# Kernel optimization log

Hardware: AMD Instinct MI355X
Metric: run time of the kernel (lower is better)

## Reference

```python
import jax, jax.numpy as jnp
import numpy as np

EPSILON = 0.05


def _l2_normalize(x, axis=1, eps=1e-12):
    return x / jnp.maximum(jnp.linalg.norm(x, axis=axis, keepdims=True), eps)


def _pairwise_euclidean_distance(a, b):
    # [N, d], [K, d] -> [N, K] euclidean distances (torch.cdist semantics)
    sq = (jnp.sum(a * a, axis=1)[:, None]
          + jnp.sum(b * b, axis=1)[None, :]
          - 2.0 * (a @ b.T))
    return jnp.sqrt(jnp.maximum(sq, 1e-12))


def _sinkhorn(out, epsilon):
    # Faithful to the original: the loop body never updates Q, so the result
    # is a single row-then-column normalization regardless of `iterations`.
    Q = jnp.exp(out / epsilon).T              # [K, B]
    K, B = Q.shape
    Q = Q / jnp.sum(Q)
    Q1 = Q / jnp.sum(Q, axis=1, keepdims=True) / K
    Q2 = Q1 / jnp.sum(Q1, axis=0, keepdims=True) / B
    return (Q2 * B).T                          # [B, K]


def _cross_entropy(x1, x2):
    return -jnp.mean(jnp.sum(x1 * jnp.log(x2), axis=1))


def setup_inputs() -> dict:
    key = jax.random.key(0)
    k1, k2, k3 = jax.random.split(key, 3)
    two_bsz, d, K = 32768, 256, 1024
    return {
        "z": jax.random.normal(k1, (two_bsz, d), dtype=jnp.float32),
        "p": jax.random.normal(k2, (two_bsz, d), dtype=jnp.float32),
        "centers": jax.random.normal(k3, (K, d), dtype=jnp.float32),
    }


def reference(z, p, centers):
    z = _l2_normalize(z, axis=1)
    p = _l2_normalize(p, axis=1)
    c = _l2_normalize(centers, axis=1)

    bsz = z.shape[0] // 2
    z1, z2 = z[:bsz], z[bsz:]
    p1, p2 = p[:bsz], p[bsz:]

    za_1 = _sinkhorn(_pairwise_euclidean_distance(z1, c), EPSILON)
    za_2 = _sinkhorn(_pairwise_euclidean_distance(z2, c), EPSILON)
    pa_1 = _sinkhorn(_pairwise_euclidean_distance(p1, c), EPSILON)
    pa_2 = _sinkhorn(_pairwise_euclidean_distance(p2, c), EPSILON)

    # cls_use_both_views = True
    return (_cross_entropy(za_1, pa_1) + _cross_entropy(za_1, pa_2)
            + _cross_entropy(za_2, pa_1) + _cross_entropy(za_2, pa_2)) / 4.0
```

## Files before the change

### kernel.cpp

```cpp
#include <hip/hip_runtime.h>
#include <math.h>

#define BH  16384
#define B2  32768
#define DIM 256
#define KC  1024

typedef __bf16 bf16x8 __attribute__((ext_vector_type(8)));
typedef float  f32x4  __attribute__((ext_vector_type(4)));

__device__ __forceinline__ unsigned short f2bf(float f) {
  unsigned int u = __float_as_uint(f);
  u += 0x7FFFu + ((u >> 16) & 1u);
  return (unsigned short)(u >> 16);
}

__device__ __forceinline__ float vsqrt(float x) {
  float r; asm("v_sqrt_f32 %0, %1" : "=v"(r) : "v"(x)); return r;
}

__device__ __forceinline__ void gld_lds16(const void* g, void* l) {
  __builtin_amdgcn_global_load_lds(
      (const __attribute__((address_space(1))) void*)g,
      (__attribute__((address_space(3))) void*)l, 16, 0, 0);
}

__global__ void norm_rows_kernel(const float* __restrict__ z,
                                 const float* __restrict__ p,
                                 const float* __restrict__ c,
                                 unsigned short* __restrict__ Xn,
                                 unsigned short* __restrict__ Cn,
                                 float* __restrict__ colsum,
                                 float* __restrict__ out) {
  if (blockIdx.x < 16) colsum[blockIdx.x * 256 + threadIdx.x] = 0.0f;
  if (blockIdx.x == 16 && threadIdx.x == 0) out[0] = 0.0f;

  int wave = threadIdx.x >> 6;
  int lane = threadIdx.x & 63;
  int row  = blockIdx.x * 4 + wave;
  const float* src; unsigned short* dst; int r;
  if (row < B2)        { src = z; dst = Xn; r = row; }
  else if (row < 2*B2) { src = p; dst = Xn + (size_t)B2 * DIM; r = row - B2; }
  else                 { src = c; dst = Cn; r = row - 2*B2; }
  float4 v = *reinterpret_cast<const float4*>(src + (size_t)r * DIM + lane * 4);
  float ss = v.x*v.x + v.y*v.y + v.z*v.z + v.w*v.w;
  #pragma unroll
  for (int m = 1; m < 64; m <<= 1) ss += __shfl_xor(ss, m);
  float inv = 1.0f / fmaxf(vsqrt(ss), 1e-12f);
  ushort4 o;
  o.x = f2bf(v.x * inv); o.y = f2bf(v.y * inv);
  o.z = f2bf(v.z * inv); o.w = f2bf(v.w * inv);
  *reinterpret_cast<ushort4*>(dst + (size_t)r * DIM + lane * 4) = o;
}

__global__ void fin_logC_kernel(const float* __restrict__ colsum,
                                float* __restrict__ logC) {
  int i = blockIdx.x * 256 + threadIdx.x;
  if (i < 4 * KC) logC[i] = 40.0f + __logf(colsum[i]);
}

__global__ __launch_bounds__(256, 2)
void gemm_s_kernel(const unsigned short* __restrict__ XA,
                   const unsigned short* __restrict__ Cn,
                   float* __restrict__ colsum,
                   unsigned char* __restrict__ S) {
  __shared__ __align__(16) char lds[65536 + 4096];
  float* lut4 = (float*)(lds + 65536);
  const int id  = blockIdx.x;
  const int xcd = id & 7, idx = id >> 3;
  const int wk  = xcd * 128 + idx;
  const int panel = wk >> 3, col = wk & 7;
  const int tm0 = panel * 128, tn0 = col * 128;

  const int tid  = threadIdx.x;
  const int lane = tid & 63;
  const int wid  = tid >> 6;
  const int wm   = wid >> 1, wn = wid & 1;
  const int l15  = lane & 15, l4 = lane >> 4;
  const int slot = tid & 3;

  int arow[4], acs[4];
  #pragma unroll
  for (int it = 0; it < 4; ++it) {
    int sl = it * 256 + tid;
    int r = sl >> 3, c = sl & 7;
    arow[it] = r;
    acs[it]  = c ^ (r & 7);
  }
  const char* Abase = (const char*)XA + (size_t)tm0 * 512;
  const char* Bbase = (const char*)Cn + (size_t)tn0 * 512;

  auto stage = [&](int t) {
    const int mat = t >> 2;
    const int bk  = t & 3;
    const int b   = t & 1;
    const char* ab = Abase + ((size_t)mat << 23);
    #pragma unroll
    for (int it = 0; it < 4; ++it) {
      gld_lds16(ab + (size_t)arow[it] * 512 + bk * 128 + acs[it] * 16,
                lds + b * 16384 + (it * 256 + tid) * 16);
      gld_lds16(Bbase + (size_t)arow[it] * 512 + bk * 128 + acs[it] * 16,
                lds + 32768 + b * 16384 + (it * 256 + tid) * 16);
    }
  };

  if (tid < 256) {
    float d = ((float)tid - 127.5f) * (1.0f / 255.0f);
    float L = 20.0f * vsqrt(2.0f - 2.0f * d);
    float v = __expf(L - 40.0f);
    ((float4*)lut4)[tid] = (float4){v, v, v, v};
  }

  f32x4 acc[4][4];
  stage(0);
  __syncthreads();

  for (int t = 0; t < 16; ++t) {
    if (t < 15) stage(t + 1);
    const int b  = t & 1;
    const int mat = t >> 2, bk = t & 3;

    if (bk == 0) {
      #pragma unroll
      for (int fi = 0; fi < 4; ++fi)
        #pragma unroll
        for (int fj = 0; fj < 4; ++fj)
          acc[fi][fj] = (f32x4){0.f, 0.f, 0.f, 0.f};
    }

    #pragma unroll
    for (int kc = 0; kc < 2; ++kc) {
      bf16x8 aF[4], bF[4];
      #pragma unroll
      for (int f = 0; f < 4; ++f) {
        const int ra = wm * 64 + f * 16 + l15;
        aF[f] = *reinterpret_cast<const bf16x8*>(
            lds + b * 16384 + ra * 128 + ((((kc << 2) | l4) ^ (ra & 7)) << 4));
        const int rb = wn * 64 + f * 16 + l15;
        bF[f] = *reinterpret_cast<const bf16x8*>(
            lds + 32768 + b * 16384 + rb * 128 + ((((kc << 2) | l4) ^ (rb & 7)) << 4));
      }
      #pragma unroll
      for (int fi = 0; fi < 4; ++fi)
        #pragma unroll
        for (int fj = 0; fj < 4; ++fj)
          acc[fi][fj] = __builtin_amdgcn_mfma_f32_16x16x32_bf16(
              aF[fi], bF[fj], acc[fi][fj], 0, 0, 0);
    }

    if (bk == 3) {
      unsigned char* Sp = S + ((size_t)mat * BH + tm0) * KC + tn0;
      #pragma unroll
      for (int fj = 0; fj < 4; ++fj) {
        float cp = 0.0f;
        #pragma unroll
        for (int fi = 0; fi < 4; ++fi)
          #pragma unroll
          for (int i = 0; i < 4; ++i) {
            float v = fmaf(acc[fi][fj][i], 255.0f, 128.0f);
            v = fminf(fmaxf(v, 0.0f), 255.0f);
            unsigned e = (unsigned)v;
            cp += lut4[(e << 2) | slot];
            int row  = wm * 64 + fi * 16 + l4 * 4 + i;
            int ccol = wn * 64 + fj * 16 + l15;
            Sp[(size_t)row * KC + ccol] = (unsigned char)e;
          }
        cp += __shfl_xor(cp, 16);
        cp += __shfl_xor(cp, 32);
        if (l4 == 0)
          atomicAdd(&colsum[mat * KC + tn0 + wn * 64 + fj * 16 + l15], cp);
      }
    }
    __syncthreads();
  }
}

__device__ __forceinline__ float decG(unsigned e, float lc) {
  float d = fmaf((float)e, 1.0f / 255.0f, -0.5f);
  float L = 20.0f * vsqrt(fmaf(-2.0f, d, 2.0f));
  return L - lc;
}

__global__ __launch_bounds__(256)
void pass2_mem_kernel(const unsigned char* __restrict__ S,
                      const float* __restrict__ logC,
                      float* __restrict__ rowv) {
  const int tid  = threadIdx.x;
  const int lane = tid & 63;
  const int wid  = tid >> 6;
  const int row  = blockIdx.x * 4 + wid;
  const size_t plane = (size_t)BH * KC;
  const unsigned char* Sr = S + (size_t)row * KC;

  float dp1 = 0.f, dp2 = 0.f, dz1 = 0.f, dz2 = 0.f, nz1 = 0.f, nz2 = 0.f;

  #pragma unroll
  for (int it = 0; it < 2; ++it) {
    const int kb = it * 512 + lane * 8;
    uint2 vz1 = *reinterpret_cast<const uint2*>(Sr + 0 * plane + kb);
    uint2 vz2 = *reinterpret_cast<const uint2*>(Sr + 1 * plane + kb);
    uint2 vp1 = *reinterpret_cast<const uint2*>(Sr + 2 * plane + kb);
    uint2 vp2 = *reinterpret_cast<const uint2*>(Sr + 3 * plane + kb);

    float cz1[8], cz2[8], cp1[8], cp2[8];
    *reinterpret_cast<float4*>(&cz1[0]) = *reinterpret_cast<const float4*>(logC + 0 * KC + kb);
    *reinterpret_cast<float4*>(&cz1[4]) = *reinterpret_cast<const float4*>(logC + 0 * KC + kb + 4);
    *reinterpret_cast<float4*>(&cz2[0]) = *reinterpret_cast<const float4*>(logC + 1 * KC + kb);
    *reinterpret_cast<float4*>(&cz2[4]) = *reinterpret_cast<const float4*>(logC + 1 * KC + kb + 4);
    *reinterpret_cast<float4*>(&cp1[0]) = *reinterpret_cast<const float4*>(logC + 2 * KC + kb);
    *reinterpret_cast<float4*>(&cp1[4]) = *reinterpret_cast<const float4*>(logC + 2 * KC + kb + 4);
    *reinterpret_cast<float4*>(&cp2[0]) = *reinterpret_cast<const float4*>(logC + 3 * KC + kb);
    *reinterpret_cast<float4*>(&cp2[4]) = *reinterpret_cast<const float4*>(logC + 3 * KC + kb + 4);

    unsigned b1[8], b2[8];
    #pragma unroll
    for (int e = 0; e < 4; ++e) {
      b1[e]     = (vp1.x >> (8 * e)) & 0xffu;
      b1[e + 4] = (vp1.y >> (8 * e)) & 0xffu;
      b2[e]     = (vp2.x >> (8 * e)) & 0xffu;
      b2[e + 4] = (vp2.y >> (8 * e)) & 0xffu;
    }
    float tv[8];
    #pragma unroll
    for (int e = 0; e < 8; ++e) {
      float g1 = decG(b1[e], cp1[e]);
      float g2 = decG(b2[e], cp2[e]);
      dp1 += __expf(g1);
      dp2 += __expf(g2);
      tv[e] = g1 + g2;
    }
    #pragma unroll
    for (int e = 0; e < 4; ++e) {
      b1[e]     = (vz1.x >> (8 * e)) & 0xffu;
      b1[e + 4] = (vz1.y >> (8 * e)) & 0xffu;
      b2[e]     = (vz2.x >> (8 * e)) & 0xffu;
      b2[e + 4] = (vz2.y >> (8 * e)) & 0xffu;
    }
    #pragma unroll
    for (int e = 0; e < 8; ++e) {
      float e1 = __expf(decG(b1[e], cz1[e]));
      float e2 = __expf(decG(b2[e], cz2[e]));
      dz1 += e1; nz1 += e1 * tv[e];
      dz2 += e2; nz2 += e2 * tv[e];
    }
  }

  #pragma unroll
  for (int m = 1; m < 64; m <<= 1) {
    dp1 += __shfl_xor(dp1, m); dp2 += __shfl_xor(dp2, m);
    dz1 += __shfl_xor(dz1, m); dz2 += __shfl_xor(dz2, m);
    nz1 += __shfl_xor(nz1, m); nz2 += __shfl_xor(nz2, m);
  }

  __shared__ float red[4];
  if (lane == 0)
    red[wid] = nz1 / dz1 + nz2 / dz2 - 2.0f * (__logf(dp1) + __logf(dp2));
  __syncthreads();
  if (tid == 0)
    rowv[blockIdx.x] = red[0] + red[1] + red[2] + red[3];
}

__global__ void fin_reduce_kernel(const float* __restrict__ rowv,
                                  float* __restrict__ out) {
  int i = blockIdx.x * 256 + threadIdx.x;
  float v = rowv[i];
  #pragma unroll
  for (int m = 1; m < 64; m <<= 1) v += __shfl_xor(v, m);
  __shared__ float ws[4];
  int lane = threadIdx.x & 63, wid = threadIdx.x >> 6;
  if (lane == 0) ws[wid] = v;
  __syncthreads();
  if (threadIdx.x == 0)
    atomicAdd(out, (ws[0] + ws[1] + ws[2] + ws[3]) * (-1.0f / 65536.0f));
}

extern "C" void kernel_launch(void* const* d_in, const int* in_sizes, int n_in,
                              void* d_out, int out_size, void* d_ws, size_t ws_size,
                              hipStream_t stream) {
  const float* z = (const float*)d_in[0];
  const float* p = (const float*)d_in[1];
  const float* c = (const float*)d_in[2];
  char* ws = (char*)d_ws;
  unsigned short* Xn = (unsigned short*)(ws);
  unsigned short* Cn = (unsigned short*)(ws + 33554432);
  float* colsum = (float*)(ws + 34078720);
  float* logC   = (float*)(ws + 34095104);
  float* rowv   = (float*)(ws + 34111488);
  unsigned char* S = (unsigned char*)(ws + 34127872);
  float* out = (float*)d_out;

  norm_rows_kernel<<<16640, 256, 0, stream>>>(z, p, c, Xn, Cn, colsum, out);
  gemm_s_kernel<<<1024, 256, 0, stream>>>(Xn, Cn, colsum, S);
  fin_logC_kernel<<<16, 256, 0, stream>>>(colsum, logC);
  pass2_mem_kernel<<<4096, 256, 0, stream>>>(S, logC, rowv);
  fin_reduce_kernel<<<16, 256, 0, stream>>>(rowv, out);
}
```

Measured before the change: 107.8 us.

## Rewrite GEMM as 256x256 tile, 8-wave kernel with interleaved load/MFMA schedule

Replaces the 128x128 four-wave GEMM with a 256x256 eight-wave kernel that uses 128KB of LDS and a hand-scheduled pipeline. Global-to-LDS loads for later tiles are interleaved with MFMA quadrants, separated by explicit barriers, sched_barriers, setprio and vmcnt waits. Larger tiles raise operand reuse and the explicit schedule aims to overlap memory traffic with matrix math. The launch drops to 256 blocks, which could leave the GPU underfilled. The manual waitcnt and barrier choreography is fragile and could hide race conditions.

```diff
diff --git a/kernel.cpp b/kernel.cpp
--- a/kernel.cpp
+++ b/kernel.cpp
@@ -59,50 +59,31 @@
   if (i < 4 * KC) logC[i] = 40.0f + __logf(colsum[i]);
 }
 
-__global__ __launch_bounds__(256, 2)
-void gemm_s_kernel(const unsigned short* __restrict__ XA,
-                   const unsigned short* __restrict__ Cn,
-                   float* __restrict__ colsum,
-                   unsigned char* __restrict__ S) {
-  __shared__ __align__(16) char lds[65536 + 4096];
-  float* lut4 = (float*)(lds + 65536);
-  const int id  = blockIdx.x;
-  const int xcd = id & 7, idx = id >> 3;
-  const int wk  = xcd * 128 + idx;
-  const int panel = wk >> 3, col = wk & 7;
-  const int tm0 = panel * 128, tn0 = col * 128;
+
+#define SBAR() __builtin_amdgcn_sched_barrier(0)
+#define BARR() __builtin_amdgcn_s_barrier()
+#define VM6()  asm volatile("s_waitcnt vmcnt(6)" ::: "memory")
+
+__global__ __launch_bounds__(512, 2)
+void gemm8_kernel(const unsigned short* __restrict__ XA,
+                  const unsigned short* __restrict__ Cn,
+                  float* __restrict__ colsum,
+                  unsigned char* __restrict__ S) {
+  __shared__ __align__(16) char lds[135168];
+  float* lut4 = (float*)(lds + 131072);
+
+  const int id = blockIdx.x;
+  const int wk = (id & 7) * 32 + (id >> 3);
+  const int panel = wk >> 2, col = wk & 3;
+  const int tm0 = panel * 256, tn0 = col * 256;
 
   const int tid  = threadIdx.x;
   const int lane = tid & 63;
   const int wid  = tid >> 6;
-  const int wm   = wid >> 1, wn = wid & 1;
+  const int wm   = wid >> 2, wn = wid & 3;
   const int l15  = lane & 15, l4 = lane >> 4;
-  const int slot = tid & 3;
-
-  int arow[4], acs[4];
-  #pragma unroll
-  for (int it = 0; it < 4; ++it) {
-    int sl = it * 256 + tid;
-    int r = sl >> 3, c = sl & 7;
-    arow[it] = r;
-    acs[it]  = c ^ (r & 7);
-  }
-  const char* Abase = (const char*)XA + (size_t)tm0 * 512;
-  const char* Bbase = (const char*)Cn + (size_t)tn0 * 512;
-
-  auto stage = [&](int t) {
-    const int mat = t >> 2;
-    const int bk  = t & 3;
-    const int b   = t & 1;
-    const char* ab = Abase + ((size_t)mat << 23);
-    #pragma unroll
-    for (int it = 0; it < 4; ++it) {
-      gld_lds16(ab + (size_t)arow[it] * 512 + bk * 128 + acs[it] * 16,
-                lds + b * 16384 + (it * 256 + tid) * 16);
-      gld_lds16(Bbase + (size_t)arow[it] * 512 + bk * 128 + acs[it] * 16,
-                lds + 32768 + b * 16384 + (it * 256 + tid) * 16);
-    }
-  };
+  const int sw   = l15 & 7;
+  const int slot4 = tid & 3;
 
   if (tid < 256) {
     float d = ((float)tid - 127.5f) * (1.0f / 255.0f);
@@ -111,57 +92,134 @@
     ((float4*)lut4)[tid] = (float4){v, v, v, v};
   }
 
-  f32x4 acc[4][4];
-  stage(0);
+  const int srow0 = tid >> 3,          sc0 = (tid & 7) ^ (srow0 & 7);
+  const int srow1 = srow0 + 64,        sc1 = ((tid + 512) & 7) ^ (srow1 & 7);
+
+#define ST_A(tile, half, dst) do {                                          \
+    int tt_ = (tile) & 15;                                                  \
+    const char* src_ = (const char*)XA + ((size_t)(tt_ >> 2) << 23)         \
+        + (size_t)(tm0 + (half) * 128) * 512 + (tt_ & 3) * 128;             \
+    gld_lds16(src_ + (size_t)srow0 * 512 + sc0 * 16,                        \
+              lds + (dst) + tid * 16);                                      \
+    gld_lds16(src_ + (size_t)srow1 * 512 + sc1 * 16,                        \
+              lds + (dst) + (tid + 512) * 16);                              \
+  } while (0)
+
+#define ST_B(tile, half, dst) do {                                          \
+    int tt_ = (tile) & 15;                                                  \
+    const char* src_ = (const char*)Cn                                      \
+        + (size_t)(tn0 + (half) * 128) * 512 + (tt_ & 3) * 128;             \
+    gld_lds16(src_ + (size_t)srow0 * 512 + sc0 * 16,                        \
+              lds + (dst) + tid * 16);                                      \
+    gld_lds16(src_ + (size_t)srow1 * 512 + sc1 * 16,                        \
+              lds + (dst) + (tid + 512) * 16);                              \
+  } while (0)
+
+  bf16x8 aR[8], bR0[4], bR1[4];
+  f32x4  acc[8][4];
+
+#define RD_A(base, ah) do {                                                 \
+    _Pragma("unroll")                                                       \
+    for (int f_ = 0; f_ < 4; ++f_) {                                        \
+      int ra_ = wm * 128 + (ah) * 64 + f_ * 16 + l15;                       \
+      _Pragma("unroll")                                                     \
+      for (int kc_ = 0; kc_ < 2; ++kc_)                                     \
+        aR[f_ * 2 + kc_] = *(const bf16x8*)(lds + (base) + ra_ * 128        \
+            + (((kc_ * 4 + l4) ^ sw) << 4));                                \
+    }                                                                       \
+  } while (0)
+
+#define RD_B(base, bh, bR) do {                                             \
+    _Pragma("unroll")                                                       \
+    for (int g_ = 0; g_ < 2; ++g_) {                                        \
+      int rb_ = wn * 64 + (bh) * 32 + g_ * 16 + l15;                        \
+      _Pragma("unroll")                                                     \
+      for (int kc_ = 0; kc_ < 2; ++kc_)                                     \
+        bR[g_ * 2 + kc_] = *(const bf16x8*)(lds + (base) + rb_ * 128        \
+            + (((kc_ * 4 + l4) ^ sw) << 4));                                \
+    }                                                                       \
+  } while (0)
+
+#define QUAD(ah, bh, bR) do {                                               \
+    _Pragma("unroll")                                                       \
+    for (int kc_ = 0; kc_ < 2; ++kc_)                                       \
+      _Pragma("unroll")                                                     \
+      for (int f_ = 0; f_ < 4; ++f_)                                        \
+        _Pragma("unroll")                                                   \
+        for (int g_ = 0; g_ < 2; ++g_)                                      \
+          acc[(ah) * 4 + f_][(bh) * 2 + g_] =                               \
+              __builtin_amdgcn_mfma_f32_16x16x32_bf16(                      \
+                  aR[f_ * 2 + kc_], bR[g_ * 2 + kc_],                       \
+                  acc[(ah) * 4 + f_][(bh) * 2 + g_], 0, 0, 0);              \
+  } while (0)
+
+#define SYNC_MFMA(ah, bh, bR) do {                                          \
+    SBAR(); BARR(); SBAR();                                                 \
+    __builtin_amdgcn_s_setprio(1);                                          \
+    QUAD(ah, bh, bR);                                                       \
+    __builtin_amdgcn_s_setprio(0);                                          \
+    SBAR(); BARR();                                                         \
+  } while (0)
+
+  ST_A(0, 0, 0);            ST_A(0, 1, 16384);
+  ST_B(0, 0, 65536);        ST_B(0, 1, 65536 + 16384);
+  ST_A(1, 0, 32768);
+  ST_B(1, 0, 65536 + 32768);
+  ST_B(1, 1, 65536 + 32768 + 16384);
   __syncthreads();
 
-  for (int t = 0; t < 16; ++t) {
-    if (t < 15) stage(t + 1);
-    const int b  = t & 1;
-    const int mat = t >> 2, bk = t & 3;
-
-    if (bk == 0) {
+  #pragma unroll 1
+  for (int it = 0; it < 8; ++it) {
+    const int t0 = 2 * it, t1 = t0 + 1;
+
+    if ((it & 1) == 0) {
       #pragma unroll
-      for (int fi = 0; fi < 4; ++fi)
+      for (int fi = 0; fi < 8; ++fi)
         #pragma unroll
         for (int fj = 0; fj < 4; ++fj)
           acc[fi][fj] = (f32x4){0.f, 0.f, 0.f, 0.f};
     }
 
-    #pragma unroll
-    for (int kc = 0; kc < 2; ++kc) {
-      bf16x8 aF[4], bF[4];
-      #pragma unroll
-      for (int f = 0; f < 4; ++f) {
-        const int ra = wm * 64 + f * 16 + l15;
-        aF[f] = *reinterpret_cast<const bf16x8*>(
-            lds + b * 16384 + ra * 128 + ((((kc << 2) | l4) ^ (ra & 7)) << 4));
-        const int rb = wn * 64 + f * 16 + l15;
-        bF[f] = *reinterpret_cast<const bf16x8*>(
-            lds + 32768 + b * 16384 + rb * 128 + ((((kc << 2) | l4) ^ (rb & 7)) << 4));
-      }
-      #pragma unroll
-      for (int fi = 0; fi < 4; ++fi)
-        #pragma unroll
-        for (int fj = 0; fj < 4; ++fj)
-          acc[fi][fj] = __builtin_amdgcn_mfma_f32_16x16x32_bf16(
-              aF[fi], bF[fj], acc[fi][fj], 0, 0, 0);
-    }
-
-    if (bk == 3) {
+    RD_B(65536, 0, bR0); RD_A(0, 0);
+    ST_A(t1, 1, 32768 + 16384);
+    SYNC_MFMA(0, 0, bR0);
+    RD_B(65536, 1, bR1);
+    ST_A(t0 + 2, 0, 0);
+    SYNC_MFMA(0, 1, bR1);
+    RD_A(0, 1);
+    ST_B(t0 + 2, 0, 65536);
+    SYNC_MFMA(1, 1, bR1);
+    ST_B(t0 + 2, 1, 65536 + 16384);
+    VM6();
+    SYNC_MFMA(1, 0, bR0);
+    RD_B(65536 + 32768, 0, bR0); RD_A(32768, 0);
+    ST_A(t0 + 2, 1, 16384);
+    SYNC_MFMA(0, 0, bR0);
+    RD_B(65536 + 32768, 1, bR1);
+    ST_A(t1 + 2, 0, 32768);
+    SYNC_MFMA(0, 1, bR1);
+    RD_A(32768, 1);
+    ST_B(t1 + 2, 0, 65536 + 32768);
+    SYNC_MFMA(1, 1, bR1);
+    ST_B(t1 + 2, 1, 65536 + 32768 + 16384);
+    VM6();
+    SYNC_MFMA(1, 0, bR0);
+
+    if (it & 1) {
+      const int mat = it >> 1;
       unsigned char* Sp = S + ((size_t)mat * BH + tm0) * KC + tn0;
       #pragma unroll
       for (int fj = 0; fj < 4; ++fj) {
         float cp = 0.0f;
         #pragma unroll
-        for (int fi = 0; fi < 4; ++fi)
+        for (int fi = 0; fi < 8; ++fi)
           #pragma unroll
           for (int i = 0; i < 4; ++i) {
             float v = fmaf(acc[fi][fj][i], 255.0f, 128.0f);
             v = fminf(fmaxf(v, 0.0f), 255.0f);
             unsigned e = (unsigned)v;
-            cp += lut4[(e << 2) | slot];
-            int row  = wm * 64 + fi * 16 + l4 * 4 + i;
+            cp += lut4[(e << 2) | slot4];
+            int row  = wm * 128 + fi * 16 + l4 * 4 + i;
             int ccol = wn * 64 + fj * 16 + l15;
             Sp[(size_t)row * KC + ccol] = (unsigned char)e;
           }
@@ -170,8 +228,8 @@
         if (l4 == 0)
           atomicAdd(&colsum[mat * KC + tn0 + wn * 64 + fj * 16 + l15], cp);
       }
-    }
-    __syncthreads();
+      VM6();
+    }
   }
 }
 
@@ -290,7 +348,7 @@
   float* out = (float*)d_out;
 
   norm_rows_kernel<<<16640, 256, 0, stream>>>(z, p, c, Xn, Cn, colsum, out);
-  gemm_s_kernel<<<1024, 256, 0, stream>>>(Xn, Cn, colsum, S);
+  gemm8_kernel<<<256, 512, 0, stream>>>(Xn, Cn, colsum, S);
   fin_logC_kernel<<<16, 256, 0, stream>>>(colsum, logC);
   pass2_mem_kernel<<<4096, 256, 0, stream>>>(S, logC, rowv);
   fin_reduce_kernel<<<16, 256, 0, stream>>>(rowv, out);
```

Result: slower. 244.5 us (+126.9%).

## Halve GEMM K-tile and LDS to raise occupancy, hoist pass2 loads

Applied to the files above, without the earlier changes.

The GEMM K-step drops from 64 to 32 elements per stage, which shrinks LDS from about 68KB to 40KB. Launch bounds rise to 4 blocks per CU to hide latency, the swizzle is adapted, and the LUT is widened to 8 slots to cut bank conflicts. In pass2, all eight byte loads per row are issued up front before the compute, to raise memory-level parallelism. The trade-off is twice as many barriers and stage steps in the GEMM, plus a tighter register budget that may cause spills.

```diff
diff --git a/kernel.cpp b/kernel.cpp
--- a/kernel.cpp
+++ b/kernel.cpp
@@ -59,13 +59,13 @@
   if (i < 4 * KC) logC[i] = 40.0f + __logf(colsum[i]);
 }
 
-__global__ __launch_bounds__(256, 2)
+__global__ __launch_bounds__(256, 4)
 void gemm_s_kernel(const unsigned short* __restrict__ XA,
                    const unsigned short* __restrict__ Cn,
                    float* __restrict__ colsum,
                    unsigned char* __restrict__ S) {
-  __shared__ __align__(16) char lds[65536 + 4096];
-  float* lut4 = (float*)(lds + 65536);
+  __shared__ __align__(16) char lds[40960];
+  float* lut8 = (float*)(lds + 32768);
   const int id  = blockIdx.x;
   const int xcd = id & 7, idx = id >> 3;
   const int wk  = xcd * 128 + idx;
@@ -77,50 +77,48 @@
   const int wid  = tid >> 6;
   const int wm   = wid >> 1, wn = wid & 1;
   const int l15  = lane & 15, l4 = lane >> 4;
-  const int slot = tid & 3;
-
-  int arow[4], acs[4];
-  #pragma unroll
-  for (int it = 0; it < 4; ++it) {
-    int sl = it * 256 + tid;
-    int r = sl >> 3, c = sl & 7;
-    arow[it] = r;
-    acs[it]  = c ^ (r & 7);
-  }
-  const char* Abase = (const char*)XA + (size_t)tm0 * 512;
-  const char* Bbase = (const char*)Cn + (size_t)tn0 * 512;
-
-  auto stage = [&](int t) {
-    const int mat = t >> 2;
-    const int bk  = t & 3;
-    const int b   = t & 1;
-    const char* ab = Abase + ((size_t)mat << 23);
-    #pragma unroll
-    for (int it = 0; it < 4; ++it) {
-      gld_lds16(ab + (size_t)arow[it] * 512 + bk * 128 + acs[it] * 16,
-                lds + b * 16384 + (it * 256 + tid) * 16);
-      gld_lds16(Bbase + (size_t)arow[it] * 512 + bk * 128 + acs[it] * 16,
-                lds + 32768 + b * 16384 + (it * 256 + tid) * 16);
-    }
-  };
-
-  if (tid < 256) {
+  const int l7   = lane & 7;
+
+  {
     float d = ((float)tid - 127.5f) * (1.0f / 255.0f);
     float L = 20.0f * vsqrt(2.0f - 2.0f * d);
     float v = __expf(L - 40.0f);
-    ((float4*)lut4)[tid] = (float4){v, v, v, v};
-  }
+    ((float4*)lut8)[tid * 2]     = (float4){v, v, v, v};
+    ((float4*)lut8)[tid * 2 + 1] = (float4){v, v, v, v};
+  }
+
+  int arow[2], acs[2];
+  #pragma unroll
+  for (int it = 0; it < 2; ++it) {
+    int slot = it * 256 + tid;
+    arow[it] = slot >> 2;
+    acs[it]  = (slot & 3) ^ (arow[it] & 3);
+  }
+  const char* Abase = (const char*)XA + (size_t)tm0 * 512;
+  const char* Bbase = (const char*)Cn + (size_t)tn0 * 512;
+
+  auto stage = [&](int t) {
+    const int mat = t >> 3, bk = t & 7, b = t & 1;
+    const char* ab = Abase + ((size_t)mat << 23);
+    #pragma unroll
+    for (int it = 0; it < 2; ++it) {
+      gld_lds16(ab + (size_t)arow[it] * 512 + bk * 64 + acs[it] * 16,
+                lds + b * 8192 + (it * 256 + tid) * 16);
+      gld_lds16(Bbase + (size_t)arow[it] * 512 + bk * 64 + acs[it] * 16,
+                lds + 16384 + b * 8192 + (it * 256 + tid) * 16);
+    }
+  };
 
   f32x4 acc[4][4];
   stage(0);
   __syncthreads();
 
-  for (int t = 0; t < 16; ++t) {
-    if (t < 15) stage(t + 1);
-    const int b  = t & 1;
-    const int mat = t >> 2, bk = t & 3;
-
-    if (bk == 0) {
+  #pragma unroll 1
+  for (int t = 0; t < 32; ++t) {
+    if (t < 31) stage(t + 1);
+    const int b = t & 1;
+
+    if ((t & 7) == 0) {
       #pragma unroll
       for (int fi = 0; fi < 4; ++fi)
         #pragma unroll
@@ -128,27 +126,25 @@
           acc[fi][fj] = (f32x4){0.f, 0.f, 0.f, 0.f};
     }
 
-    #pragma unroll
-    for (int kc = 0; kc < 2; ++kc) {
-      bf16x8 aF[4], bF[4];
+    bf16x8 aF[4], bF[4];
+    #pragma unroll
+    for (int f = 0; f < 4; ++f) {
+      const int ra = wm * 64 + f * 16 + l15;
+      aF[f] = *reinterpret_cast<const bf16x8*>(
+          lds + b * 8192 + ra * 64 + ((l4 ^ (ra & 3)) << 4));
+      const int rb = wn * 64 + f * 16 + l15;
+      bF[f] = *reinterpret_cast<const bf16x8*>(
+          lds + 16384 + b * 8192 + rb * 64 + ((l4 ^ (rb & 3)) << 4));
+    }
+    #pragma unroll
+    for (int fi = 0; fi < 4; ++fi)
       #pragma unroll
-      for (int f = 0; f < 4; ++f) {
-        const int ra = wm * 64 + f * 16 + l15;
-        aF[f] = *reinterpret_cast<const bf16x8*>(
-            lds + b * 16384 + ra * 128 + ((((kc << 2) | l4) ^ (ra & 7)) << 4));
-        const int rb = wn * 64 + f * 16 + l15;
-        bF[f] = *reinterpret_cast<const bf16x8*>(
-            lds + 32768 + b * 16384 + rb * 128 + ((((kc << 2) | l4) ^ (rb & 7)) << 4));
-      }
-      #pragma unroll
-      for (int fi = 0; fi < 4; ++fi)
-        #pragma unroll
-        for (int fj = 0; fj < 4; ++fj)
-          acc[fi][fj] = __builtin_amdgcn_mfma_f32_16x16x32_bf16(
-              aF[fi], bF[fj], acc[fi][fj], 0, 0, 0);
-    }
-
-    if (bk == 3) {
+      for (int fj = 0; fj < 4; ++fj)
+        acc[fi][fj] = __builtin_amdgcn_mfma_f32_16x16x32_bf16(
+            aF[fi], bF[fj], acc[fi][fj], 0, 0, 0);
+
+    if ((t & 7) == 7) {
+      const int mat = t >> 3;
       unsigned char* Sp = S + ((size_t)mat * BH + tm0) * KC + tn0;
       #pragma unroll
       for (int fj = 0; fj < 4; ++fj) {
@@ -160,7 +156,7 @@
             float v = fmaf(acc[fi][fj][i], 255.0f, 128.0f);
             v = fminf(fmaxf(v, 0.0f), 255.0f);
             unsigned e = (unsigned)v;
-            cp += lut4[(e << 2) | slot];
+            cp += lut8[(e << 3) | l7];
             int row  = wm * 64 + fi * 16 + l4 * 4 + i;
             int ccol = wn * 64 + fj * 16 + l15;
             Sp[(size_t)row * KC + ccol] = (unsigned char)e;
@@ -190,18 +186,20 @@
   const int wid  = tid >> 6;
   const int row  = blockIdx.x * 4 + wid;
   const size_t plane = (size_t)BH * KC;
-  const unsigned char* Sr = S + (size_t)row * KC;
+  const unsigned char* Sr = S + (size_t)row * KC + lane * 8;
+
+  uint2 vz1a = *reinterpret_cast<const uint2*>(Sr + 0 * plane);
+  uint2 vz1b = *reinterpret_cast<const uint2*>(Sr + 0 * plane + 512);
+  uint2 vz2a = *reinterpret_cast<const uint2*>(Sr + 1 * plane);
+  uint2 vz2b = *reinterpret_cast<const uint2*>(Sr + 1 * plane + 512);
+  uint2 vp1a = *reinterpret_cast<const uint2*>(Sr + 2 * plane);
+  uint2 vp1b = *reinterpret_cast<const uint2*>(Sr + 2 * plane + 512);
+  uint2 vp2a = *reinterpret_cast<const uint2*>(Sr + 3 * plane);
+  uint2 vp2b = *reinterpret_cast<const uint2*>(Sr + 3 * plane + 512);
 
   float dp1 = 0.f, dp2 = 0.f, dz1 = 0.f, dz2 = 0.f, nz1 = 0.f, nz2 = 0.f;
 
-  #pragma unroll
-  for (int it = 0; it < 2; ++it) {
-    const int kb = it * 512 + lane * 8;
-    uint2 vz1 = *reinterpret_cast<const uint2*>(Sr + 0 * plane + kb);
-    uint2 vz2 = *reinterpret_cast<const uint2*>(Sr + 1 * plane + kb);
-    uint2 vp1 = *reinterpret_cast<const uint2*>(Sr + 2 * plane + kb);
-    uint2 vp2 = *reinterpret_cast<const uint2*>(Sr + 3 * plane + kb);
-
+  auto doit = [&](uint2 vz1, uint2 vz2, uint2 vp1, uint2 vp2, int kb) {
     float cz1[8], cz2[8], cp1[8], cp2[8];
     *reinterpret_cast<float4*>(&cz1[0]) = *reinterpret_cast<const float4*>(logC + 0 * KC + kb);
     *reinterpret_cast<float4*>(&cz1[4]) = *reinterpret_cast<const float4*>(logC + 0 * KC + kb + 4);
@@ -243,7 +241,10 @@
       dz1 += e1; nz1 += e1 * tv[e];
       dz2 += e2; nz2 += e2 * tv[e];
     }
-  }
+  };
+
+  doit(vz1a, vz2a, vp1a, vp2a, lane * 8);
+  doit(vz1b, vz2b, vp1b, vp2b, 512 + lane * 8);
 
   #pragma unroll
   for (int m = 1; m < 64; m <<= 1) {
```

After: 192.9 us. 1.79x slower.

## Use partial vmcnt waits with raw barriers and hoist pass2 byte loads

Applied to the files above, without the earlier changes.

In the GEMM/quantize kernel, the loop is fully unrolled and each __syncthreads is replaced by an explicit s_waitcnt vmcnt(8) plus s_barrier wrapped in sched_barriers. This lets the next stage's global-to-LDS loads stay in flight while the current tile is consumed, and the trailing barrier is skipped on the last iteration. In pass2, all eight byte-plane loads are issued up front, before any compute, to raise memory-level parallelism. The hand-tuned vmcnt count assumes the exact number of loads issued per stage, so a miscount could cause LDS races.

```diff
diff --git a/kernel.cpp b/kernel.cpp
--- a/kernel.cpp
+++ b/kernel.cpp
@@ -115,8 +115,18 @@
   stage(0);
   __syncthreads();
 
+  #pragma unroll
   for (int t = 0; t < 16; ++t) {
-    if (t < 15) stage(t + 1);
+    if (t < 15) {
+      stage(t + 1);
+      asm volatile("s_waitcnt vmcnt(8)" ::: "memory");
+    } else {
+      asm volatile("s_waitcnt vmcnt(0)" ::: "memory");
+    }
+    __builtin_amdgcn_sched_barrier(0);
+    __builtin_amdgcn_s_barrier();
+    __builtin_amdgcn_sched_barrier(0);
+
     const int b  = t & 1;
     const int mat = t >> 2, bk = t & 3;
 
@@ -171,7 +181,12 @@
           atomicAdd(&colsum[mat * KC + tn0 + wn * 64 + fj * 16 + l15], cp);
       }
     }
-    __syncthreads();
+
+    if (t < 15) {
+      __builtin_amdgcn_sched_barrier(0);
+      __builtin_amdgcn_s_barrier();
+      __builtin_amdgcn_sched_barrier(0);
+    }
   }
 }
 
@@ -190,18 +205,20 @@
   const int wid  = tid >> 6;
   const int row  = blockIdx.x * 4 + wid;
   const size_t plane = (size_t)BH * KC;
-  const unsigned char* Sr = S + (size_t)row * KC;
+  const unsigned char* Sr = S + (size_t)row * KC + lane * 8;
+
+  uint2 vz1a = *reinterpret_cast<const uint2*>(Sr + 0 * plane);
+  uint2 vz1b = *reinterpret_cast<const uint2*>(Sr + 0 * plane + 512);
+  uint2 vz2a = *reinterpret_cast<const uint2*>(Sr + 1 * plane);
+  uint2 vz2b = *reinterpret_cast<const uint2*>(Sr + 1 * plane + 512);
+  uint2 vp1a = *reinterpret_cast<const uint2*>(Sr + 2 * plane);
+  uint2 vp1b = *reinterpret_cast<const uint2*>(Sr + 2 * plane + 512);
+  uint2 vp2a = *reinterpret_cast<const uint2*>(Sr + 3 * plane);
+  uint2 vp2b = *reinterpret_cast<const uint2*>(Sr + 3 * plane + 512);
 
   float dp1 = 0.f, dp2 = 0.f, dz1 = 0.f, dz2 = 0.f, nz1 = 0.f, nz2 = 0.f;
 
-  #pragma unroll
-  for (int it = 0; it < 2; ++it) {
-    const int kb = it * 512 + lane * 8;
-    uint2 vz1 = *reinterpret_cast<const uint2*>(Sr + 0 * plane + kb);
-    uint2 vz2 = *reinterpret_cast<const uint2*>(Sr + 1 * plane + kb);
-    uint2 vp1 = *reinterpret_cast<const uint2*>(Sr + 2 * plane + kb);
-    uint2 vp2 = *reinterpret_cast<const uint2*>(Sr + 3 * plane + kb);
-
+  auto doit = [&](uint2 vz1, uint2 vz2, uint2 vp1, uint2 vp2, int kb) {
     float cz1[8], cz2[8], cp1[8], cp2[8];
     *reinterpret_cast<float4*>(&cz1[0]) = *reinterpret_cast<const float4*>(logC + 0 * KC + kb);
     *reinterpret_cast<float4*>(&cz1[4]) = *reinterpret_cast<const float4*>(logC + 0 * KC + kb + 4);
@@ -243,7 +260,10 @@
       dz1 += e1; nz1 += e1 * tv[e];
       dz2 += e2; nz2 += e2 * tv[e];
     }
-  }
+  };
+
+  doit(vz1a, vz2a, vp1a, vp2a, lane * 8);
+  doit(vz1b, vz2b, vp1b, vp2b, 512 + lane * 8);
 
   #pragma unroll
   for (int m = 1; m < 64; m <<= 1) {
```

Result: slower. 132.1 us (+22.6%).
